# Kernel tuning notes

Measured on AMD Instinct MI355X. Metric: run time of the kernel, lower is better.

The kernel has to match this reference:

```python
import jax, jax.numpy as jnp
import numpy as np

B, N, DIM = 4, 2048, 1024
HEADS, DIM_HEAD = 16, 64
INNER = HEADS * DIM_HEAD  # 1024
SCALE = DIM_HEAD ** -0.5

def setup_inputs() -> dict:
    key = jax.random.key(0)
    k1, k2, k3 = jax.random.split(key, 3)
    x = jax.random.normal(k1, (B, N, DIM), dtype=jnp.float32)
    w_qkv = jax.random.normal(k2, (DIM, 3 * INNER), dtype=jnp.float32) * (DIM ** -0.5)
    w_out = jax.random.normal(k3, (INNER, DIM), dtype=jnp.float32) * (INNER ** -0.5)
    b_out = jnp.zeros((DIM,), dtype=jnp.float32)
    return {"x": x, "w_qkv": w_qkv, "w_out": w_out, "b_out": b_out}

def reference(x, w_qkv, w_out, b_out):
    b, n, _ = x.shape
    qkv = x @ w_qkv  # [b, n, 3*inner]
    q, k, v = jnp.split(qkv, 3, axis=-1)
    # [b, n, h, d] -> [b, h, n, d]
    reshape = lambda t: t.reshape(b, n, HEADS, DIM_HEAD).transpose(0, 2, 1, 3)
    q, k, v = reshape(q), reshape(k), reshape(v)
    dots = jnp.einsum('bhqd,bhkd->bhqk', q, k) * SCALE
    attn = jax.nn.softmax(dots, axis=-1)
    out = jnp.einsum('bhqk,bhkd->bhqd', attn, v)
    out = out.transpose(0, 2, 1, 3).reshape(b, n, INNER)
    return out @ w_out + b_out
```

## Files before the change

### kernel.cpp

```cpp
#include <hip/hip_runtime.h>

typedef unsigned short u16;
typedef __bf16 bf16_t;
typedef bf16_t bf16x8 __attribute__((ext_vector_type(8)));
typedef float f32x4 __attribute__((ext_vector_type(4)));
typedef float f32x16 __attribute__((ext_vector_type(16)));
typedef u16 u16x8 __attribute__((ext_vector_type(8)));
typedef u16 u16x4 __attribute__((ext_vector_type(4)));
typedef unsigned uint2v __attribute__((ext_vector_type(2)));

#define B_     4
#define N_     2048
#define DIM_   1024
#define HEADS_ 16
#define DH_    64
#define INNER_ 1024
#define QKV3_  3072
#define SCALE_ 0.125f
#define LOG2E_ 1.44269504089f

__device__ __forceinline__ u16 f2bf(float f) {
  union { float f; unsigned u; } v; v.f = f;
  unsigned r = v.u + 0x7FFFu + ((v.u >> 16) & 1u);
  return (u16)(r >> 16);
}
__device__ __forceinline__ u16 bfbits(float f) {
  bf16_t b = (bf16_t)f;
  return __builtin_bit_cast(u16, b);
}
__device__ __forceinline__ unsigned packbf(float lo, float hi) {
  return (unsigned)bfbits(lo) | ((unsigned)bfbits(hi) << 16);
}

#if __has_builtin(__builtin_amdgcn_exp2f)
#define EXP2F(x) __builtin_amdgcn_exp2f(x)
#else
#define EXP2F(x) __expf((x) * 0.69314718056f)
#endif

typedef __attribute__((address_space(1))) const unsigned int ga_u32;
typedef __attribute__((address_space(3))) unsigned int ls_u32;
__device__ __forceinline__ void gload16(const void* g, void* l) {
  __builtin_amdgcn_global_load_lds((ga_u32*)g, (ls_u32*)l, 16, 0, 0);
}

__global__ __launch_bounds__(256) void cvt_f32_bf16(const float* __restrict__ in,
                                                    u16* __restrict__ out, int n8) {
  int i = blockIdx.x * 256 + threadIdx.x;
  if (i < n8) {
    const float4* p = (const float4*)(in + (size_t)i * 8);
    float4 a = p[0], b = p[1];
    u16x8 o;
    o[0] = f2bf(a.x); o[1] = f2bf(a.y); o[2] = f2bf(a.z); o[3] = f2bf(a.w);
    o[4] = f2bf(b.x); o[5] = f2bf(b.y); o[6] = f2bf(b.z); o[7] = f2bf(b.w);
    *(u16x8*)(out + (size_t)i * 8) = o;
  }
}

__global__ __launch_bounds__(256) void transp_w(const float* __restrict__ in,
                                                u16* __restrict__ out, int Kd, int Nd) {
  __shared__ float t[32][33];
  int n0 = blockIdx.x * 32, k0 = blockIdx.y * 32;
  int tx = threadIdx.x & 31, ty = threadIdx.x >> 5;
#pragma unroll
  for (int i = 0; i < 4; i++)
    t[ty + i * 8][tx] = in[(size_t)(k0 + ty + i * 8) * Nd + n0 + tx];
  __syncthreads();
#pragma unroll
  for (int i = 0; i < 4; i++)
    out[(size_t)(n0 + ty + i * 8) * Kd + k0 + tx] = f2bf(t[tx][ty + i * 8]);
}

__global__ __launch_bounds__(256) void transp_v(const u16* __restrict__ qkv,
                                                u16* __restrict__ vT) {
  __shared__ u16 t[32][33];
  int bh = blockIdx.z; int b = bh >> 4, h = bh & 15;
  int n0 = blockIdx.x * 32, d0 = blockIdx.y * 32;
  int tx = threadIdx.x & 31, ty = threadIdx.x >> 5;
#pragma unroll
  for (int i = 0; i < 4; i++)
    t[ty + i * 8][tx] =
        qkv[(size_t)(b * N_ + n0 + ty + i * 8) * QKV3_ + 2 * INNER_ + h * DH_ + d0 + tx];
  __syncthreads();
#pragma unroll
  for (int i = 0; i < 4; i++)
    vT[((size_t)bh * DH_ + d0 + ty + i * 8) * N_ + n0 + tx] = t[tx][ty + i * 8];
}

template <int F32OUT>
__global__ __launch_bounds__(256) void gemm_bt(const u16* __restrict__ A,
                                               const u16* __restrict__ BT,
                                               void* __restrict__ Cp,
                                               const float* __restrict__ bias,
                                               int M, int N, int K) {
  __shared__ alignas(16) u16 ldsA[2][128 * 64];
  __shared__ alignas(16) u16 ldsB[2][128 * 64];
  const int tid = threadIdx.x;
  const int lane = tid & 63, wid = tid >> 6;
  const int l16 = lane & 15, lg = lane >> 4;

  int bid = blockIdx.x;
  const int cpx = gridDim.x >> 3;
  bid = (bid & 7) * cpx + (bid >> 3);

  const int ntiles = N >> 7;
  const int tm = bid / ntiles, tn = bid % ntiles;
  const int m0 = tm << 7, n0 = tn << 7;
  const int wr = wid >> 1, wc = wid & 1;

  const int srow_in = lane >> 3;
  const int soff = ((lane & 7) ^ srow_in) * 8;

  f32x4 acc[4][4];
#pragma unroll
  for (int i = 0; i < 4; i++)
#pragma unroll
    for (int j = 0; j < 4; j++) acc[i][j] = f32x4{0.f, 0.f, 0.f, 0.f};

  const int KSTEPS = K >> 6;

#define GSTAGE_(kk, buf)                                                           \
  do {                                                                             \
    const int k1_ = (kk) << 6;                                                     \
    char* bA_ = (char*)&ldsA[(buf)][0];                                            \
    char* bB_ = (char*)&ldsB[(buf)][0];                                            \
    _Pragma("unroll")                                                              \
    for (int i_ = 0; i_ < 4; i_++) {                                               \
      const int rb_ = wid * 32 + i_ * 8;                                           \
      gload16(A  + (size_t)(m0 + rb_ + srow_in) * K + k1_ + soff, bA_ + rb_ * 128);\
      gload16(BT + (size_t)(n0 + rb_ + srow_in) * K + k1_ + soff, bB_ + rb_ * 128);\
    }                                                                              \
  } while (0)

  GSTAGE_(0, 0);
  GSTAGE_(1, 1);

  for (int ks = 0; ks < KSTEPS; ks++) {
    if (ks + 1 < KSTEPS) asm volatile("s_waitcnt vmcnt(8)" ::: "memory");
    else                 asm volatile("s_waitcnt vmcnt(0)" ::: "memory");
    __builtin_amdgcn_s_barrier();

    const char* cA = (const char*)&ldsA[ks & 1][0];
    const char* cB = (const char*)&ldsB[ks & 1][0];

    bf16x8 bf[4][2];
#pragma unroll
    for (int n = 0; n < 4; n++) {
      int row = wc * 64 + n * 16 + l16;
      int rb = row * 128, swz = (row & 7) << 4;
      bf[n][0] = *(const bf16x8*)(cB + rb + ((lg * 16) ^ swz));
      bf[n][1] = *(const bf16x8*)(cB + rb + ((64 + lg * 16) ^ swz));
    }
    __builtin_amdgcn_s_setprio(1);
#pragma unroll
    for (int mm = 0; mm < 4; mm++) {
      int row = wr * 64 + mm * 16 + l16;
      int rb = row * 128, swz = (row & 7) << 4;
      bf16x8 af0 = *(const bf16x8*)(cA + rb + ((lg * 16) ^ swz));
      bf16x8 af1 = *(const bf16x8*)(cA + rb + ((64 + lg * 16) ^ swz));
#pragma unroll
      for (int n = 0; n < 4; n++) {
        acc[mm][n] = __builtin_amdgcn_mfma_f32_16x16x32_bf16(af0, bf[n][0], acc[mm][n], 0, 0, 0);
        acc[mm][n] = __builtin_amdgcn_mfma_f32_16x16x32_bf16(af1, bf[n][1], acc[mm][n], 0, 0, 0);
      }
    }
    __builtin_amdgcn_s_setprio(0);

    __builtin_amdgcn_s_barrier();
    if (ks + 2 < KSTEPS) GSTAGE_(ks + 2, ks & 1);
  }
#undef GSTAGE_

#pragma unroll
  for (int mm = 0; mm < 4; mm++) {
#pragma unroll
    for (int n = 0; n < 4; n++) {
      int row = m0 + wr * 64 + mm * 16 + lg * 4;
      int col = n0 + wc * 64 + n * 16 + l16;
#pragma unroll
      for (int j = 0; j < 4; j++) {
        if (F32OUT)
          ((float*)Cp)[(size_t)(row + j) * N + col] = acc[mm][n][j] + bias[col];
        else
          ((u16*)Cp)[(size_t)(row + j) * N + col] = f2bf(acc[mm][n][j]);
      }
    }
  }
}

__global__ __launch_bounds__(512, 4) void attn_fwd(const u16* __restrict__ qkv,
                                                   const u16* __restrict__ vT,
                                                   u16* __restrict__ abuf) {
  __shared__ alignas(16) u16 ldsK[3][64 * 64];
  __shared__ alignas(16) u16 ldsV[3][64 * 64];

  const int tid = threadIdx.x;
  const int lane = tid & 63, wid = tid >> 6;
  const int l32 = lane & 31, hl = lane >> 5;

  int bid = blockIdx.x;
  bid = (bid & 7) * 64 + (bid >> 3);
  const int bh = bid >> 3, qt = bid & 7;
  const int b = bh >> 4, h = bh & 15;
  const int q0 = qt * 256 + wid * 32;

  constexpr float QS = SCALE_ * LOG2E_;
  bf16x8 qf[4];
  {
    const u16* qrow = qkv + (size_t)(b * N_ + q0 + l32) * QKV3_ + h * DH_ + hl * 8;
#pragma unroll
    for (int step = 0; step < 4; step++) {
      bf16x8 t = *(const bf16x8*)(qrow + step * 16);
#pragma unroll
      for (int i = 0; i < 8; i++) t[i] = (bf16_t)((float)t[i] * QS);
      qf[step] = t;
    }
  }

  const int srow = tid >> 3;
  const int sswz = (tid & 7) ^ (srow & 7);
  const u16* ksrc = qkv + (size_t)(b * N_ + srow) * QKV3_ + INNER_ + h * DH_ + sswz * 8;
  const u16* vsrc = vT + ((size_t)bh * DH_ + srow) * N_ + sswz * 8;
  const int sdst = wid << 10;

  float lrow = 0.f;
  f32x16 acc[2];
#pragma unroll
  for (int i = 0; i < 16; i++) { acc[0][i] = 0.f; acc[1][i] = 0.f; }

  gload16(ksrc, (char*)ldsK + sdst);
  gload16(vsrc, (char*)ldsV + sdst);
  gload16(ksrc + (size_t)64 * QKV3_, (char*)ldsK + 8192 + sdst);
  gload16(vsrc + 64, (char*)ldsV + 8192 + sdst);

  const int NT = N_ / 64;
  int cur = 0, pre = 2;

  for (int kt = 0; kt < NT; ++kt) {
    if (kt < NT - 1) asm volatile("s_waitcnt vmcnt(2)" ::: "memory");
    else             asm volatile("s_waitcnt vmcnt(0)" ::: "memory");
    __builtin_amdgcn_s_barrier();
    if (kt + 2 < NT) {
      gload16(ksrc + (size_t)(kt + 2) * 64 * QKV3_, (char*)ldsK + pre * 8192 + sdst);
      gload16(vsrc + (kt + 2) * 64, (char*)ldsV + pre * 8192 + sdst);
    }

    const char* Kb = (const char*)ldsK + cur * 8192;
    const char* Vb = (const char*)ldsV + cur * 8192;

    f32x16 s[2];
    __builtin_amdgcn_s_setprio(1);
#pragma unroll
    for (int ktile = 0; ktile < 2; ktile++) {
      f32x16 c;
#pragma unroll
      for (int i = 0; i < 16; i++) c[i] = 0.f;
      const int r = ktile * 32 + l32;
      const char* rb = Kb + r * 128;
      const int swz = (r & 7) << 4;
#pragma unroll
      for (int step = 0; step < 4; step++) {
        bf16x8 kf = *(const bf16x8*)(rb + ((step * 32 + hl * 16) ^ swz));
        c = __builtin_amdgcn_mfma_f32_32x32x16_bf16(kf, qf[step], c, 0, 0, 0);
      }
      s[ktile] = c;
    }
    __builtin_amdgcn_s_setprio(0);

    float ps0 = 0.f, ps1 = 0.f;
#pragma unroll
    for (int ktile = 0; ktile < 2; ktile++)
#pragma unroll
      for (int i = 0; i < 16; i += 2) {
        const float p0 = EXP2F(s[ktile][i]);
        const float p1 = EXP2F(s[ktile][i + 1]);
        s[ktile][i] = p0; s[ktile][i + 1] = p1;
        ps0 += p0; ps1 += p1;
      }
    lrow += ps0 + ps1;

    bf16x8 pb[4];
#pragma unroll
    for (int ktile = 0; ktile < 2; ktile++)
#pragma unroll
      for (int par = 0; par < 2; par++) {
        const int rb8 = par * 8;
        const unsigned c0 = packbf(s[ktile][rb8 + 0], s[ktile][rb8 + 1]);
        const unsigned c1 = packbf(s[ktile][rb8 + 2], s[ktile][rb8 + 3]);
        const unsigned c2 = packbf(s[ktile][rb8 + 4], s[ktile][rb8 + 5]);
        const unsigned c3 = packbf(s[ktile][rb8 + 6], s[ktile][rb8 + 7]);
        const uint2v r02 = __builtin_amdgcn_permlane32_swap(c0, c2, false, false);
        const uint2v r13 = __builtin_amdgcn_permlane32_swap(c1, c3, false, false);
        union { unsigned u[4]; bf16x8 v; } w;
        w.u[0] = r02[0]; w.u[1] = r13[0]; w.u[2] = r02[1]; w.u[3] = r13[1];
        pb[ktile * 2 + par] = w.v;
      }

    __builtin_amdgcn_s_setprio(1);
#pragma unroll
    for (int dtile = 0; dtile < 2; dtile++) {
      const int r = dtile * 32 + l32;
      const char* rb = Vb + r * 128;
      const int swz = (r & 7) << 4;
      f32x16 c = acc[dtile];
#pragma unroll
      for (int step = 0; step < 4; step++) {
        bf16x8 vf = *(const bf16x8*)(rb + ((step * 32 + hl * 16) ^ swz));
        c = __builtin_amdgcn_mfma_f32_32x32x16_bf16(vf, pb[step], c, 0, 0, 0);
      }
      acc[dtile] = c;
    }
    __builtin_amdgcn_s_setprio(0);

    cur = (cur == 2) ? 0 : cur + 1;
    pre = (pre == 2) ? 0 : pre + 1;
  }

  lrow += __shfl_xor(lrow, 32);
  const float inv = 1.f / lrow;
  const size_t row = (size_t)(b * N_ + q0 + l32);
#pragma unroll
  for (int dtile = 0; dtile < 2; dtile++)
#pragma unroll
    for (int g = 0; g < 4; g++) {
      u16x4 w;
#pragma unroll
      for (int j = 0; j < 4; j++) w[j] = bfbits(acc[dtile][g * 4 + j] * inv);
      const int d = dtile * 32 + g * 8 + hl * 4;
      *(u16x4*)(abuf + row * INNER_ + h * DH_ + d) = w;
    }
}

extern "C" void kernel_launch(void* const* d_in, const int* in_sizes, int n_in,
                              void* d_out, int out_size, void* d_ws, size_t ws_size,
                              hipStream_t stream) {
  const float* x     = (const float*)d_in[0];
  const float* w_qkv = (const float*)d_in[1];
  const float* w_out = (const float*)d_in[2];
  const float* b_out = (const float*)d_in[3];
  float* out = (float*)d_out;

  char* ws = (char*)d_ws;
  u16* xb    = (u16*)(ws);
  u16* wqkvT = (u16*)(ws + (size_t)(16 << 20));
  u16* woutT = (u16*)(ws + (size_t)(22 << 20));
  u16* qkv   = (u16*)(ws + (size_t)(24 << 20));
  u16* vTb   = (u16*)(ws + (size_t)(72 << 20));
  u16* abuf  = xb;

  cvt_f32_bf16<<<4096, 256, 0, stream>>>(x, xb, (B_ * N_ * DIM_) / 8);
  transp_w<<<dim3(QKV3_ / 32, DIM_ / 32), 256, 0, stream>>>(w_qkv, wqkvT, DIM_, QKV3_);
  transp_w<<<dim3(DIM_ / 32, INNER_ / 32), 256, 0, stream>>>(w_out, woutT, INNER_, DIM_);
  gemm_bt<0><<<(B_ * N_ / 128) * (QKV3_ / 128), 256, 0, stream>>>(
      xb, wqkvT, qkv, nullptr, B_ * N_, QKV3_, DIM_);
  transp_v<<<dim3(N_ / 32, DH_ / 32, B_ * HEADS_), 256, 0, stream>>>(qkv, vTb);
  attn_fwd<<<512, 512, 0, stream>>>(qkv, vTb, abuf);
  gemm_bt<1><<<(B_ * N_ / 128) * (DIM_ / 128), 256, 0, stream>>>(
      abuf, woutT, out, b_out, B_ * N_, DIM_, INNER_);
}
```

Baseline: 195.3 us.

## Pre-tile K and V into MFMA fragment layout for contiguous attention loads

Adds a ktile_prep kernel and changes transp_v so that K and V are written into per-64-key tiles already ordered to match the MFMA operand fragment layout. The attention kernel can then stream each tile with fully contiguous 16-byte loads and read LDS with simple linear offsets, with no XOR swizzle. This removes strided global reads of K rows and the swizzle arithmetic. In exchange it adds an extra kernel launch and a pass over K, uses the output buffer as scratch, and the new linear LDS pattern may cause bank conflicts.

```diff
diff --git a/kernel.cpp b/kernel.cpp
--- a/kernel.cpp
+++ b/kernel.cpp
@@ -71,8 +71,23 @@
     out[(size_t)(n0 + ty + i * 8) * Kd + k0 + tx] = f2bf(t[tx][ty + i * 8]);
 }
 
+__global__ __launch_bounds__(256) void ktile_prep(const u16* __restrict__ qkv,
+                                                  u16* __restrict__ ktiled) {
+  const int blk = blockIdx.x;
+  const int bh = blk >> 5, kt = blk & 31;
+  const int b = bh >> 4, h = bh & 15;
+  const int tid = threadIdx.x;
+  const int s = tid & 7, r0 = tid >> 3;
+  const u16* src = qkv + (size_t)(b * N_ + kt * 64 + r0) * QKV3_ + INNER_ + h * DH_ + s * 8;
+  u16* dst = ktiled + (size_t)blk * 4096 + s * 512 + r0 * 8;
+  uint4 v0 = *(const uint4*)(src);
+  uint4 v1 = *(const uint4*)(src + (size_t)32 * QKV3_);
+  *(uint4*)(dst) = v0;
+  *(uint4*)(dst + 256) = v1;
+}
+
 __global__ __launch_bounds__(256) void transp_v(const u16* __restrict__ qkv,
-                                                u16* __restrict__ vT) {
+                                                u16* __restrict__ vtiled) {
   __shared__ u16 t[32][33];
   int bh = blockIdx.z; int b = bh >> 4, h = bh & 15;
   int n0 = blockIdx.x * 32, d0 = blockIdx.y * 32;
@@ -82,9 +97,12 @@
     t[ty + i * 8][tx] =
         qkv[(size_t)(b * N_ + n0 + ty + i * 8) * QKV3_ + 2 * INNER_ + h * DH_ + d0 + tx];
   __syncthreads();
-#pragma unroll
-  for (int i = 0; i < 4; i++)
-    vT[((size_t)bh * DH_ + d0 + ty + i * 8) * N_ + n0 + tx] = t[tx][ty + i * 8];
+  const int n = n0 + tx;
+  u16* obase = vtiled + (size_t)bh * 131072 + (size_t)(n >> 6) * 4096 +
+               ((n >> 3) & 7) * 512 + (n & 7);
+#pragma unroll
+  for (int i = 0; i < 4; i++)
+    obase[(d0 + ty + i * 8) * 8] = t[tx][ty + i * 8];
 }
 
 template <int F32OUT>
@@ -189,7 +207,8 @@
 }
 
 __global__ __launch_bounds__(512, 4) void attn_fwd(const u16* __restrict__ qkv,
-                                                   const u16* __restrict__ vT,
+                                                   const u16* __restrict__ ktiled,
+                                                   const u16* __restrict__ vtiled,
                                                    u16* __restrict__ abuf) {
   __shared__ alignas(16) u16 ldsK[3][64 * 64];
   __shared__ alignas(16) u16 ldsV[3][64 * 64];
@@ -217,21 +236,21 @@
     }
   }
 
-  const int srow = tid >> 3;
-  const int sswz = (tid & 7) ^ (srow & 7);
-  const u16* ksrc = qkv + (size_t)(b * N_ + srow) * QKV3_ + INNER_ + h * DH_ + sswz * 8;
-  const u16* vsrc = vT + ((size_t)bh * DH_ + srow) * N_ + sswz * 8;
+  const u16* kts = ktiled + (size_t)bh * 131072 + tid * 8;
+  const u16* vts = vtiled + (size_t)bh * 131072 + tid * 8;
   const int sdst = wid << 10;
+
+  const int kofs = (hl << 10) + (l32 << 4);
 
   float lrow = 0.f;
   f32x16 acc[2];
 #pragma unroll
   for (int i = 0; i < 16; i++) { acc[0][i] = 0.f; acc[1][i] = 0.f; }
 
-  gload16(ksrc, (char*)ldsK + sdst);
-  gload16(vsrc, (char*)ldsV + sdst);
-  gload16(ksrc + (size_t)64 * QKV3_, (char*)ldsK + 8192 + sdst);
-  gload16(vsrc + 64, (char*)ldsV + 8192 + sdst);
+  gload16(kts, (char*)ldsK + sdst);
+  gload16(vts, (char*)ldsV + sdst);
+  gload16(kts + 4096, (char*)ldsK + 8192 + sdst);
+  gload16(vts + 4096, (char*)ldsV + 8192 + sdst);
 
   const int NT = N_ / 64;
   int cur = 0, pre = 2;
@@ -241,8 +260,8 @@
     else             asm volatile("s_waitcnt vmcnt(0)" ::: "memory");
     __builtin_amdgcn_s_barrier();
     if (kt + 2 < NT) {
-      gload16(ksrc + (size_t)(kt + 2) * 64 * QKV3_, (char*)ldsK + pre * 8192 + sdst);
-      gload16(vsrc + (kt + 2) * 64, (char*)ldsV + pre * 8192 + sdst);
+      gload16(kts + (size_t)(kt + 2) * 4096, (char*)ldsK + pre * 8192 + sdst);
+      gload16(vts + (size_t)(kt + 2) * 4096, (char*)ldsV + pre * 8192 + sdst);
     }
 
     const char* Kb = (const char*)ldsK + cur * 8192;
@@ -255,12 +274,10 @@
       f32x16 c;
 #pragma unroll
       for (int i = 0; i < 16; i++) c[i] = 0.f;
-      const int r = ktile * 32 + l32;
-      const char* rb = Kb + r * 128;
-      const int swz = (r & 7) << 4;
+      const char* rb = Kb + (ktile << 9) + kofs;
 #pragma unroll
       for (int step = 0; step < 4; step++) {
-        bf16x8 kf = *(const bf16x8*)(rb + ((step * 32 + hl * 16) ^ swz));
+        bf16x8 kf = *(const bf16x8*)(rb + (step << 11));
         c = __builtin_amdgcn_mfma_f32_32x32x16_bf16(kf, qf[step], c, 0, 0, 0);
       }
       s[ktile] = c;
@@ -299,13 +316,11 @@
     __builtin_amdgcn_s_setprio(1);
 #pragma unroll
     for (int dtile = 0; dtile < 2; dtile++) {
-      const int r = dtile * 32 + l32;
-      const char* rb = Vb + r * 128;
-      const int swz = (r & 7) << 4;
+      const char* rb = Vb + (dtile << 9) + kofs;
       f32x16 c = acc[dtile];
 #pragma unroll
       for (int step = 0; step < 4; step++) {
-        bf16x8 vf = *(const bf16x8*)(rb + ((step * 32 + hl * 16) ^ swz));
+        bf16x8 vf = *(const bf16x8*)(rb + (step << 11));
         c = __builtin_amdgcn_mfma_f32_32x32x16_bf16(vf, pb[step], c, 0, 0, 0);
       }
       acc[dtile] = c;
@@ -341,20 +356,22 @@
   float* out = (float*)d_out;
 
   char* ws = (char*)d_ws;
-  u16* xb    = (u16*)(ws);
-  u16* wqkvT = (u16*)(ws + (size_t)(16 << 20));
-  u16* woutT = (u16*)(ws + (size_t)(22 << 20));
-  u16* qkv   = (u16*)(ws + (size_t)(24 << 20));
-  u16* vTb   = (u16*)(ws + (size_t)(72 << 20));
-  u16* abuf  = xb;
+  u16* xb     = (u16*)(ws);
+  u16* wqkvT  = (u16*)(ws + (size_t)(16 << 20));
+  u16* woutT  = (u16*)(ws + (size_t)(22 << 20));
+  u16* qkv    = (u16*)(ws + (size_t)(24 << 20));
+  u16* vtiled = (u16*)(ws + (size_t)(72 << 20));
+  u16* ktiled = (u16*)d_out;
+  u16* abuf   = xb;
 
   cvt_f32_bf16<<<4096, 256, 0, stream>>>(x, xb, (B_ * N_ * DIM_) / 8);
   transp_w<<<dim3(QKV3_ / 32, DIM_ / 32), 256, 0, stream>>>(w_qkv, wqkvT, DIM_, QKV3_);
   transp_w<<<dim3(DIM_ / 32, INNER_ / 32), 256, 0, stream>>>(w_out, woutT, INNER_, DIM_);
   gemm_bt<0><<<(B_ * N_ / 128) * (QKV3_ / 128), 256, 0, stream>>>(
       xb, wqkvT, qkv, nullptr, B_ * N_, QKV3_, DIM_);
-  transp_v<<<dim3(N_ / 32, DH_ / 32, B_ * HEADS_), 256, 0, stream>>>(qkv, vTb);
-  attn_fwd<<<512, 512, 0, stream>>>(qkv, vTb, abuf);
+  ktile_prep<<<B_ * HEADS_ * 32, 256, 0, stream>>>(qkv, ktiled);
+  transp_v<<<dim3(N_ / 32, DH_ / 32, B_ * HEADS_), 256, 0, stream>>>(qkv, vtiled);
+  attn_fwd<<<512, 512, 0, stream>>>(qkv, ktiled, vtiled, abuf);
   gemm_bt<1><<<(B_ * N_ / 128) * (DIM_ / 128), 256, 0, stream>>>(
       abuf, woutT, out, b_out, B_ * N_, DIM_, INNER_);
 }
```

After: 200.7 us. 1.03x slower.
